# Kernel tuning notes

Measured on AMD Instinct MI355X. Metric: run time of the kernel, lower is better.

## Reference

```python
import jax, jax.numpy as jnp
import numpy as np

B = 256          # users (batch)
F_PER = 64       # friends per user (uniform so split/pad == reshape)
L = 50           # per-friend history length (softmax axis)
D = 128          # embed dim
N = B * F_PER    # total friend rows


def setup_inputs() -> dict:
    key = jax.random.key(0)
    k1, k2, k3 = jax.random.split(key, 3)
    friend_diff_x = jax.random.normal(k1, (N, L, D), dtype=jnp.float32)
    self_x = jax.random.normal(k2, (B, D), dtype=jnp.float32)
    friend_num_src = F_PER  # python int split size (uniform counts)
    friend_num_src_tensor = jnp.full((B,), F_PER, dtype=jnp.int64)
    friend_diff_src_mask = jax.random.randint(k3, (N, L), 0, 2) > 0
    return {
        "friend_diff_x": friend_diff_x,
        "self_x": self_x,
        "friend_num_src": friend_num_src,
        "friend_num_src_tensor": friend_num_src_tensor,
        "friend_diff_src_mask": friend_diff_src_mask,
    }


def reference(friend_diff_x, self_x, friend_num_src, friend_num_src_tensor, friend_diff_src_mask):
    # repeat_interleave with uniform counts == static jnp.repeat
    rep = jnp.repeat(self_x, friend_num_src, axis=0)              # [N, D]
    # bmm([N,L,D] x [N,D,1]) -> [N,L] dot-product scores
    scores = jnp.einsum("nld,nd->nl", friend_diff_x, rep)         # [N, L]
    w = jax.nn.softmax(scores, axis=-1)[..., None]                 # [N, L, 1]
    m = friend_diff_src_mask[..., None].astype(friend_diff_x.dtype)
    # softmax-weighted, masked sum over history -> [N, D]
    pooled = jnp.sum(w * friend_diff_x * m, axis=1)
    # split by (uniform) friend counts + pad_sequence == reshape
    return pooled.reshape(self_x.shape[0], friend_num_src, -1)    # [B, F, D]
```

## Files before the change

### kernel.cpp

```cpp
#include <hip/hip_runtime.h>
#include <math.h>

constexpr int B_ = 256;
constexpr int F_ = 64;
constexpr int L_ = 50;
constexpr int D_ = 128;
constexpr int N_ = B_ * F_;

typedef float f32x4 __attribute__((ext_vector_type(4)));

__global__ __launch_bounds__(256) void FRIENDATTN_67680094650650_kernel(
    const float* __restrict__ x,
    const float* __restrict__ selfx,
    const int* __restrict__ mask,
    float* __restrict__ out)
{
    __shared__ __align__(16) float xs[L_ * D_];
    __shared__ float score_s[L_];
    __shared__ float w_s[L_];

    const int tid = threadIdx.x;
    const int n = blockIdx.x;
    const int b = n >> 6;

    const int dq = (tid & 31) * 4;
    const f32x4 sf = *(const f32x4*)(selfx + b * D_ + dq);

    const float* xrow = x + (size_t)n * (L_ * D_);
    for (int c = tid; c < (L_ * D_) / 4; c += 256) {
        *(f32x4*)(xs + c * 4) = *(const f32x4*)(xrow + c * 4);
    }
    __syncthreads();

    {
        const int lsub = tid >> 5;
        for (int l = lsub; l < L_; l += 8) {
            f32x4 v = *(const f32x4*)(xs + l * D_ + dq);
            float acc = v.x * sf.x + v.y * sf.y + v.z * sf.z + v.w * sf.w;
#pragma unroll
            for (int off = 16; off >= 1; off >>= 1)
                acc += __shfl_xor(acc, off);
            if ((tid & 31) == 0) score_s[l] = acc;
        }
    }
    __syncthreads();

    if (tid < 64) {
        const int l = tid;
        float s = (l < L_) ? score_s[l] : -INFINITY;
        float m = s;
#pragma unroll
        for (int off = 32; off >= 1; off >>= 1) m = fmaxf(m, __shfl_xor(m, off));
        float e = (l < L_) ? __expf(s - m) : 0.f;
        float sum = e;
#pragma unroll
        for (int off = 32; off >= 1; off >>= 1) sum += __shfl_xor(sum, off);
        if (l < L_) {
            int mk = mask[(size_t)n * L_ + l];
            w_s[l] = mk ? (e / sum) : 0.f;
        }
    }
    __syncthreads();

    if (tid < D_) {
        float acc = 0.f;
#pragma unroll
        for (int l = 0; l < L_; ++l) acc += w_s[l] * xs[l * D_ + tid];
        out[(size_t)n * D_ + tid] = acc;
    }
}

extern "C" void kernel_launch(void* const* d_in, const int* in_sizes, int n_in,
                              void* d_out, int out_size, void* d_ws, size_t ws_size,
                              hipStream_t stream) {
    const float* x     = (const float*)d_in[0];
    const float* selfx = (const float*)d_in[1];
    const int*   mask  = (const int*)d_in[4];
    float*       out   = (float*)d_out;

    FRIENDATTN_67680094650650_kernel<<<N_, 256, 0, stream>>>(x, selfx, mask, out);
}
```

Before: 549.1 us.

## Keep friend history rows in registers instead of staging through LDS

Each thread now loads its slice of the 50x128 history tile directly into registers (up to 7 float4s), computes the dot-product scores from registers, and does the weighted pooling from the same registers. Partial sums are reduced across half-waves by shuffle and across waves through a small shared buffer. This drops the 25 KB shared-memory staging, letting more blocks fit per CU for latency hiding, and spreads the pooling across all 256 threads instead of 128. The mask load is also issued early so it overlaps the main loads. The cost is higher register pressure and an extra sync and reduction step.

```diff
diff --git a/kernel.cpp b/kernel.cpp
--- a/kernel.cpp
+++ b/kernel.cpp
@@ -15,33 +15,42 @@
     const int* __restrict__ mask,
     float* __restrict__ out)
 {
-    __shared__ __align__(16) float xs[L_ * D_];
     __shared__ float score_s[L_];
     __shared__ float w_s[L_];
+    __shared__ __align__(16) float pool[4][D_];
 
     const int tid = threadIdx.x;
-    const int n = blockIdx.x;
-    const int b = n >> 6;
-
-    const int dq = (tid & 31) * 4;
-    const f32x4 sf = *(const f32x4*)(selfx + b * D_ + dq);
+    const int n   = blockIdx.x;
+    const int b   = n >> 6;
+    const int g   = tid >> 5;
+    const int r   = tid & 31;
+    const int dc  = r * 4;
 
     const float* xrow = x + (size_t)n * (L_ * D_);
-    for (int c = tid; c < (L_ * D_) / 4; c += 256) {
-        *(f32x4*)(xs + c * 4) = *(const f32x4*)(xrow + c * 4);
+
+    f32x4 v[7];
+#pragma unroll
+    for (int k = 0; k < 6; ++k)
+        v[k] = *(const f32x4*)(xrow + (size_t)(tid + 256 * k) * 4);
+    const bool has7 = tid < 64;
+    if (has7) v[6] = *(const f32x4*)(xrow + (size_t)(tid + 1536) * 4);
+
+    const f32x4 sf = *(const f32x4*)(selfx + b * D_ + dc);
+    int mk = 1;
+    if (tid < L_) mk = mask[(size_t)n * L_ + tid];
+
+#pragma unroll
+    for (int k = 0; k < 6; ++k) {
+        float acc = v[k].x * sf.x + v[k].y * sf.y + v[k].z * sf.z + v[k].w * sf.w;
+#pragma unroll
+        for (int off = 16; off >= 1; off >>= 1) acc += __shfl_xor(acc, off);
+        if (r == 0) score_s[g + 8 * k] = acc;
     }
-    __syncthreads();
-
-    {
-        const int lsub = tid >> 5;
-        for (int l = lsub; l < L_; l += 8) {
-            f32x4 v = *(const f32x4*)(xs + l * D_ + dq);
-            float acc = v.x * sf.x + v.y * sf.y + v.z * sf.z + v.w * sf.w;
+    if (has7) {
+        float acc = v[6].x * sf.x + v[6].y * sf.y + v[6].z * sf.z + v[6].w * sf.w;
 #pragma unroll
-            for (int off = 16; off >= 1; off >>= 1)
-                acc += __shfl_xor(acc, off);
-            if ((tid & 31) == 0) score_s[l] = acc;
-        }
+        for (int off = 16; off >= 1; off >>= 1) acc += __shfl_xor(acc, off);
+        if (r == 0) score_s[g + 48] = acc;
     }
     __syncthreads();
 
@@ -55,18 +64,31 @@
         float sum = e;
 #pragma unroll
         for (int off = 32; off >= 1; off >>= 1) sum += __shfl_xor(sum, off);
-        if (l < L_) {
-            int mk = mask[(size_t)n * L_ + l];
-            w_s[l] = mk ? (e / sum) : 0.f;
-        }
+        if (l < L_) w_s[l] = mk ? (e / sum) : 0.f;
     }
     __syncthreads();
 
+    f32x4 p = {0.f, 0.f, 0.f, 0.f};
+#pragma unroll
+    for (int k = 0; k < 6; ++k) {
+        const float wl = w_s[g + 8 * k];
+        p.x += wl * v[k].x; p.y += wl * v[k].y;
+        p.z += wl * v[k].z; p.w += wl * v[k].w;
+    }
+    if (has7) {
+        const float wl = w_s[g + 48];
+        p.x += wl * v[6].x; p.y += wl * v[6].y;
+        p.z += wl * v[6].z; p.w += wl * v[6].w;
+    }
+    p.x += __shfl_xor(p.x, 32); p.y += __shfl_xor(p.y, 32);
+    p.z += __shfl_xor(p.z, 32); p.w += __shfl_xor(p.w, 32);
+    const int wv = tid >> 6;
+    if ((tid & 63) < 32) *(f32x4*)(&pool[wv][dc]) = p;
+    __syncthreads();
+
     if (tid < D_) {
-        float acc = 0.f;
-#pragma unroll
-        for (int l = 0; l < L_; ++l) acc += w_s[l] * xs[l * D_ + tid];
-        out[(size_t)n * D_ + tid] = acc;
+        out[(size_t)n * D_ + tid] =
+            pool[0][tid] + pool[1][tid] + pool[2][tid] + pool[3][tid];
     }
 }
 
```

New measurement: 543.1 us. About the same (-1.1%).
